# Optimization experiments

Hardware: AMD Instinct MI355X
Metric: run time of the kernel (lower is better)

The kernel has to match this reference:

```python
import jax, jax.numpy as jnp
import numpy as np

C = 256          # in_channels
CQK = C // 8     # query/key channels


def setup_inputs() -> dict:
    key = jax.random.key(0)
    ks = jax.random.split(key, 10)
    B, H, W = 4, 64, 64
    x1 = jax.random.normal(ks[0], (B, C, H, W), dtype=jnp.float32)
    x2 = jax.random.normal(ks[1], (B, C, H, W), dtype=jnp.float32)
    s = 0.05
    Wq = jax.random.normal(ks[2], (CQK, C), dtype=jnp.float32) * s
    bq = jax.random.normal(ks[3], (CQK,), dtype=jnp.float32) * s
    Wk = jax.random.normal(ks[4], (CQK, C), dtype=jnp.float32) * s
    bk = jax.random.normal(ks[5], (CQK,), dtype=jnp.float32) * s
    Wv = jax.random.normal(ks[6], (C, C), dtype=jnp.float32) * s
    bv = jax.random.normal(ks[7], (C,), dtype=jnp.float32) * s
    Wc = jax.random.normal(ks[8], (C, 2 * C), dtype=jnp.float32) * s
    bc = jax.random.normal(ks[9], (C,), dtype=jnp.float32) * s
    return {"x1": x1, "x2": x2, "Wq": Wq, "bq": bq, "Wk": Wk, "bk": bk,
            "Wv": Wv, "bv": bv, "Wc": Wc, "bc": bc}


def _proj(x_flat, Wm, b):
    # 1x1 conv == channel GEMM: [B,C,N] -> [B,Cout,N]
    return jnp.einsum('oc,bcn->bon', Wm, x_flat) + b[None, :, None]


def reference(x1, x2, Wq, bq, Wk, bk, Wv, bv, Wc, bc):
    B, Cin, H, W = x1.shape
    N = H * W
    xf1 = x1.reshape(B, Cin, N)
    xf2 = x2.reshape(B, Cin, N)
    q1 = _proj(xf1, Wq, bq)   # [B,CQK,N]
    k1 = _proj(xf1, Wk, bk)
    v1 = _proj(xf1, Wv, bv)   # [B,C,N]
    q2 = _proj(xf2, Wq, bq)
    k2 = _proj(xf2, Wk, bk)
    v2 = _proj(xf2, Wv, bv)

    def branch(q, k, v_other):
        # attn[b,i,j] = softmax_j(q[:, :, i] . k[:, :, j])
        attn = jax.nn.softmax(jnp.einsum('bci,bcj->bij', q, k), axis=2)
        # attended[b,c,i] = sum_j v_other[b,c,j] * attn[b,i,j]
        return jnp.einsum('bcj,bij->bci', v_other, attn)

    att1 = branch(q1, k1, v2).reshape(B, Cin, H, W)
    att2 = branch(q2, k2, v1).reshape(B, Cin, H, W)

    def combine(a, b_att):
        cat = jnp.concatenate((a, b_att), axis=1).reshape(B, 2 * Cin, N)
        comb = (jnp.einsum('oc,bcn->bon', Wc, cat) + bc[None, :, None]).reshape(B, Cin, H, W)
        return jnp.abs(comb).sum(axis=1, keepdims=True)

    # NOTE: original code uses x1 in BOTH combines (faithful to source)
    out1 = combine(x1, att1)
    out2 = combine(x1, att2)
    return out1, out2
```

## Files before the change

kernel.cpp:

```cpp
#include <hip/hip_runtime.h>
#include <cstdint>

#define LOG2E 1.4426950408889634f

typedef __bf16 bf16x8 __attribute__((ext_vector_type(8)));
typedef float f32x4 __attribute__((ext_vector_type(4)));

#define MFMA16(a,b,c) __builtin_amdgcn_mfma_f32_16x16x32_bf16((a),(b),(c),0,0,0)

#define LDS_BARRIER() asm volatile("s_waitcnt lgkmcnt(0)\n\ts_barrier" ::: "memory")

constexpr size_t OFF_XT = 0;
constexpr size_t OFF_QT = 8388608;
constexpr size_t OFF_KT = 9437184;
constexpr size_t OFF_V  = 10485760;
constexpr size_t OFF_WQ = 18874368;
constexpr size_t OFF_WK = 18882560;
constexpr size_t OFF_WV = 18890752;
constexpr size_t OFF_WC = 18956288;

static __device__ __forceinline__ unsigned short f2b(float a) {
  return __builtin_bit_cast(unsigned short, (__bf16)a);
}
static __device__ __forceinline__ unsigned pk2(float a, float b) {
  return ((unsigned)f2b(b) << 16) | (unsigned)f2b(a);
}

__global__ __launch_bounds__(256) void prep_kernel(
    const float* __restrict__ x1, const float* __restrict__ x2,
    const float* __restrict__ Wq, const float* __restrict__ Wk,
    const float* __restrict__ Wv, const float* __restrict__ Wc,
    short* __restrict__ ws)
{
  __shared__ float tile[64][65];
  const int tid = threadIdx.x;
  const int blk = blockIdx.x;
  if (blk < 2048) {
    const int nt = blk & 63, ct = (blk >> 6) & 3, b = (blk >> 8) & 3, inp = blk >> 10;
    const float* x = (inp ? x2 : x1) + (size_t)(b * 256 + ct * 64) * 4096 + nt * 64;
#pragma unroll
    for (int p = 0; p < 4; ++p) {
      int r = p * 16 + (tid >> 4);
      float4 v = *(const float4*)(x + (size_t)r * 4096 + (tid & 15) * 4);
      tile[r][(tid & 15) * 4 + 0] = v.x;
      tile[r][(tid & 15) * 4 + 1] = v.y;
      tile[r][(tid & 15) * 4 + 2] = v.z;
      tile[r][(tid & 15) * 4 + 3] = v.w;
    }
    __syncthreads();
    const int n = tid >> 2, c0 = (tid & 3) * 16;
    unsigned u[8];
#pragma unroll
    for (int k = 0; k < 8; ++k)
      u[k] = pk2(tile[c0 + 2 * k][n], tile[c0 + 2 * k + 1][n]);
    short* dst = ws + OFF_XT + (size_t)((inp * 4 + b) * 4096 + nt * 64 + n) * 256 + ct * 64 + c0;
    uint4 s0; s0.x = u[0]; s0.y = u[1]; s0.z = u[2]; s0.w = u[3];
    uint4 s1; s1.x = u[4]; s1.y = u[5]; s1.z = u[6]; s1.w = u[7];
    *(uint4*)(dst) = s0;
    *(uint4*)(dst + 8) = s1;
  } else {
    int idx = (blk - 2048) * 4096 + tid * 16;
    const float* src; short* dst; int off;
    if (idx < 8192)        { src = Wq; dst = ws + OFF_WQ; off = idx; }
    else if (idx < 16384)  { src = Wk; dst = ws + OFF_WK; off = idx - 8192; }
    else if (idx < 81920)  { src = Wv; dst = ws + OFF_WV; off = idx - 16384; }
    else                   { src = Wc; dst = ws + OFF_WC; off = idx - 81920; }
#pragma unroll
    for (int j = 0; j < 16; ++j) dst[off + j] = (short)f2b(src[off + j]);
  }
}

__global__ __launch_bounds__(256) void proj_qk_kernel(
    short* __restrict__ ws, const float* __restrict__ bq, const float* __restrict__ bk)
{
  const int tid = threadIdx.x, lane = tid & 63, wid = tid >> 6;
  const int g = lane >> 4, l15 = lane & 15;
  const int blk = blockIdx.x;
  const int nt = blk & 31, b = (blk >> 5) & 3, inp = blk >> 7;
  const int n0 = nt * 128 + wid * 32;

  const short* xp  = ws + OFF_XT + (size_t)(inp * 4 + b) * (4096 * 256) + (size_t)n0 * 256;
  const short* wqp = ws + OFF_WQ;
  const short* wkp = ws + OFF_WK;
  short* Qt = ws + OFF_QT + (size_t)(inp * 4 + b) * (4096 * 32);
  short* Kt = ws + OFF_KT + (size_t)(inp * 4 + b) * (4096 * 32);

  const f32x4 z4 = {0.f, 0.f, 0.f, 0.f};
  f32x4 aq[2][2], ak[2][2];
#pragma unroll
  for (int i = 0; i < 2; ++i)
#pragma unroll
    for (int j = 0; j < 2; ++j) { aq[i][j] = z4; ak[i][j] = z4; }

#pragma unroll
  for (int ks = 0; ks < 8; ++ks) {
    bf16x8 xa[2];
#pragma unroll
    for (int ns = 0; ns < 2; ++ns)
      xa[ns] = *(const bf16x8*)(xp + (size_t)(ns * 16 + l15) * 256 + ks * 32 + g * 8);
#pragma unroll
    for (int os = 0; os < 2; ++os) {
      bf16x8 wq8 = *(const bf16x8*)(wqp + (size_t)(os * 16 + l15) * 256 + ks * 32 + g * 8);
      bf16x8 wk8 = *(const bf16x8*)(wkp + (size_t)(os * 16 + l15) * 256 + ks * 32 + g * 8);
#pragma unroll
      for (int ns = 0; ns < 2; ++ns) {
        aq[ns][os] = MFMA16(xa[ns], wq8, aq[ns][os]);
        ak[ns][os] = MFMA16(xa[ns], wk8, ak[ns][os]);
      }
    }
  }
  float bqv[2], bkv[2];
#pragma unroll
  for (int os = 0; os < 2; ++os) { bqv[os] = bq[os * 16 + l15]; bkv[os] = bk[os * 16 + l15]; }
#pragma unroll
  for (int ns = 0; ns < 2; ++ns)
#pragma unroll
    for (int os = 0; os < 2; ++os)
#pragma unroll
      for (int r = 0; r < 4; ++r) {
        int n = n0 + ns * 16 + g * 4 + r;
        int o = os * 16 + l15;
        Qt[(size_t)n * 32 + o] = (short)f2b((aq[ns][os][r] + bqv[os]) * LOG2E);
        Kt[(size_t)n * 32 + o] = (short)f2b(ak[ns][os][r] + bkv[os]);
      }
}

__global__ __launch_bounds__(256) void proj_v_kernel(
    short* __restrict__ ws, const float* __restrict__ bv)
{
  const int tid = threadIdx.x, lane = tid & 63, wid = tid >> 6;
  const int g = lane >> 4, l15 = lane & 15;
  const int blk = blockIdx.x;
  const int nt = blk & 63, b = (blk >> 6) & 3, inp = blk >> 8;
  const int n0 = nt * 64;

  const short* xp  = ws + OFF_XT + (size_t)(inp * 4 + b) * (4096 * 256) + (size_t)n0 * 256;
  const short* wvp = ws + OFF_WV;
  short* Vp = ws + OFF_V + (size_t)(inp * 4 + b) * (256 * 4096);

  __shared__ __align__(16) char vl[32768];

  const f32x4 z4 = {0.f, 0.f, 0.f, 0.f};
  f32x4 acc[4][4];
#pragma unroll
  for (int i = 0; i < 4; ++i)
#pragma unroll
    for (int j = 0; j < 4; ++j) acc[i][j] = z4;

#pragma unroll
  for (int ks = 0; ks < 8; ++ks) {
    bf16x8 xa[4];
#pragma unroll
    for (int ns = 0; ns < 4; ++ns)
      xa[ns] = *(const bf16x8*)(xp + (size_t)(ns * 16 + l15) * 256 + ks * 32 + g * 8);
#pragma unroll
    for (int os = 0; os < 4; ++os) {
      bf16x8 wv8 = *(const bf16x8*)(wvp + (size_t)(wid * 64 + os * 16 + l15) * 256 + ks * 32 + g * 8);
#pragma unroll
      for (int ns = 0; ns < 4; ++ns)
        acc[os][ns] = MFMA16(wv8, xa[ns], acc[os][ns]);
    }
  }
  float bvv[4][4];
#pragma unroll
  for (int os = 0; os < 4; ++os)
#pragma unroll
    for (int r = 0; r < 4; ++r) bvv[os][r] = bv[wid * 64 + os * 16 + g * 4 + r];

  char* myl = vl + wid * 8192;
#pragma unroll
  for (int os = 0; os < 4; ++os)
#pragma unroll
    for (int ns = 0; ns < 4; ++ns)
#pragma unroll
      for (int r = 0; r < 4; ++r) {
        int o_loc = os * 16 + g * 4 + r;
        int n_loc = ns * 16 + l15;
        *(short*)(myl + o_loc * 128 + ((n_loc * 2) ^ ((o_loc & 7) << 4))) =
            (short)f2b(acc[os][ns][r] + bvv[os][r]);
      }
#pragma unroll
  for (int sc = 0; sc < 4; ++sc)
#pragma unroll
    for (int sj = 0; sj < 2; ++sj) {
      int c_loc = sc * 16 + l15;
      bf16x8 row = *(const bf16x8*)(myl + c_loc * 128 +
                                    (((unsigned)(sj * 64 + g * 16)) ^ ((c_loc & 7) << 4)));
      size_t c16 = (size_t)(wid * 4 + sc);
      size_t j32 = (size_t)(nt * 2 + sj);
      *(bf16x8*)(Vp + (c16 * 128 + j32) * 512 + lane * 8) = row;
    }
}

__global__ __launch_bounds__(256, 2) void attn_kernel(
    short* __restrict__ ws, const float* __restrict__ bc, float* __restrict__ out)
{
  const int tid = threadIdx.x, lane = tid & 63, wid = tid >> 6;
  const int g = lane >> 4, l15 = lane & 15;
  const int blk = blockIdx.x;
  const int itile = blk & 63, b = (blk >> 6) & 3, br = blk >> 8;
  const int i0 = itile * 64;

  __shared__ __align__(16) char sm[34048];
  float* l_l  = (float*)(sm + 32768);
  float* part = (float*)(sm + 33024);

  const short* Qb  = ws + OFF_QT + (size_t)(br * 4 + b) * (4096 * 32);
  const short* Kb  = ws + OFF_KT + (size_t)(br * 4 + b) * (4096 * 32);
  const short* Vb  = ws + OFF_V  + (size_t)((1 - br) * 4 + b) * (256 * 4096);
  const short* xb  = ws + OFF_XT + (size_t)b * (4096 * 256);
  const short* Wcb = ws + OFF_WC;

  const f32x4 z4 = {0.f, 0.f, 0.f, 0.f};

  bf16x8 qf = *(const bf16x8*)(Qb + (size_t)(i0 + wid * 16 + l15) * 32 + g * 8);

  f32x4 oc[4][4];
#pragma unroll
  for (int i = 0; i < 4; ++i)
#pragma unroll
    for (int j = 0; j < 4; ++j) oc[i][j] = z4;
  float l_run = 0.f;

  bf16x8 kf[2][4], va[2][2][4];
#pragma unroll
  for (int jt = 0; jt < 4; ++jt)
    kf[0][jt] = *(const bf16x8*)(Kb + (size_t)(jt * 16 + l15) * 32 + g * 8);
#pragma unroll
  for (int ks = 0; ks < 2; ++ks)
#pragma unroll
    for (int cs = 0; cs < 4; ++cs)
      va[0][ks][cs] = *(const bf16x8*)(Vb + ((size_t)(wid * 4 + cs) * 128 + ks) * 512 + lane * 8);

#define ATTN_BODY(tcur, CUR, NXT, tnxt, PB)                                              \
  do {                                                                                   \
    f32x4 st[4];                                                                         \
    _Pragma("unroll")                                                                    \
    for (int jt = 0; jt < 4; ++jt) st[jt] = MFMA16(kf[CUR][jt], qf, z4);                 \
    _Pragma("unroll")                                                                    \
    for (int jt = 0; jt < 4; ++jt)                                                       \
      kf[NXT][jt] = *(const bf16x8*)(Kb + (size_t)((tnxt) * 64 + jt * 16 + l15) * 32 + g * 8); \
    _Pragma("unroll")                                                                    \
    for (int ks = 0; ks < 2; ++ks)                                                       \
      _Pragma("unroll")                                                                  \
      for (int cs = 0; cs < 4; ++cs)                                                     \
        va[NXT][ks][cs] = *(const bf16x8*)(Vb + ((size_t)(wid * 4 + cs) * 128 +          \
                                                 (size_t)(tnxt) * 2 + ks) * 512 + lane * 8); \
    _Pragma("unroll")                                                                    \
    for (int jt = 0; jt < 4; ++jt)                                                       \
      _Pragma("unroll")                                                                  \
      for (int r = 0; r < 4; ++r) {                                                      \
        float p = exp2f(st[jt][r]);                                                      \
        st[jt][r] = p;                                                                   \
        l_run += p;                                                                      \
      }                                                                                  \
    {                                                                                    \
      char* Pl = sm + (PB) * 8192;                                                       \
      int irow = wid * 16 + l15;                                                         \
      unsigned sw = (unsigned)((irow & 7) << 4);                                         \
      _Pragma("unroll")                                                                  \
      for (int jt = 0; jt < 4; ++jt) {                                                   \
        unsigned long long u =                                                           \
            ((unsigned long long)pk2(st[jt][2], st[jt][3]) << 32) | pk2(st[jt][0], st[jt][1]); \
        *(unsigned long long*)(Pl + irow * 128 + (((unsigned)(jt * 32 + g * 8)) ^ sw)) = u; \
      }                                                                                  \
    }                                                                                    \
    LDS_BARRIER();                                                                       \
    {                                                                                    \
      const char* Pl = sm + (PB) * 8192;                                                 \
      _Pragma("unroll")                                                                  \
      for (int ks = 0; ks < 2; ++ks)                                                     \
        _Pragma("unroll")                                                                \
        for (int it = 0; it < 4; ++it) {                                                 \
          int i = it * 16 + l15;                                                         \
          bf16x8 pb = *(const bf16x8*)(Pl + i * 128 +                                    \
                                       (((unsigned)(ks * 64 + g * 16)) ^ ((i & 7) << 4))); \
          _Pragma("unroll")                                                              \
          for (int cs = 0; cs < 4; ++cs)                                                 \
            oc[cs][it] = MFMA16(va[CUR][ks][cs], pb, oc[cs][it]);                        \
        }                                                                                \
    }                                                                                    \
  } while (0)

  for (int t = 0; t < 64; t += 2) {
    ATTN_BODY(t, 0, 1, t + 1, 0);
    ATTN_BODY(t + 1, 1, 0, (t + 2 < 64) ? (t + 2) : 63, 1);
  }
#undef ATTN_BODY

  l_run += __shfl_xor(l_run, 16);
  l_run += __shfl_xor(l_run, 32);

  if (g == 0) l_l[wid * 16 + l15] = l_run;
  __syncthreads();
  float rl[4];
#pragma unroll
  for (int it = 0; it < 4; ++it) rl[it] = 1.f / l_l[it * 16 + l15];

#pragma unroll
  for (int cs = 0; cs < 4; ++cs)
#pragma unroll
    for (int it = 0; it < 4; ++it) {
      f32x4 v = oc[cs][it];
      v *= rl[it];
      int i = it * 16 + l15;
      unsigned byte = (unsigned)(i * 512) +
                      (((unsigned)((wid * 64 + cs * 16 + g * 4) * 2)) ^ ((i & 7) << 4));
      unsigned long long u = ((unsigned long long)pk2(v[2], v[3]) << 32) | pk2(v[0], v[1]);
      *(unsigned long long*)(sm + byte) = u;
    }
  __syncthreads();

  f32x4 cc[4][4];
#pragma unroll
  for (int i = 0; i < 4; ++i)
#pragma unroll
    for (int j = 0; j < 4; ++j) cc[i][j] = z4;

#pragma unroll
  for (int ks = 0; ks < 16; ++ks) {
    bf16x8 bfr[4];
#pragma unroll
    for (int ns = 0; ns < 4; ++ns) {
      int n = ns * 16 + l15;
      if (ks < 8)
        bfr[ns] = *(const bf16x8*)(xb + (size_t)(i0 + n) * 256 + ks * 32 + g * 8);
      else
        bfr[ns] = *(const bf16x8*)(sm + n * 512 +
                                   (((unsigned)((ks - 8) * 64 + g * 16)) ^ ((n & 7) << 4)));
    }
#pragma unroll
    for (int os = 0; os < 4; ++os) {
      bf16x8 af = *(const bf16x8*)(Wcb + (size_t)(wid * 64 + os * 16 + l15) * 512 + ks * 32 + g * 8);
#pragma unroll
      for (int ns = 0; ns < 4; ++ns)
        cc[os][ns] = MFMA16(af, bfr[ns], cc[os][ns]);
    }
  }
  float bcv[4][4];
#pragma unroll
  for (int os = 0; os < 4; ++os)
#pragma unroll
    for (int r = 0; r < 4; ++r) bcv[os][r] = bc[wid * 64 + os * 16 + g * 4 + r];

#pragma unroll
  for (int ns = 0; ns < 4; ++ns) {
    float tsum = 0.f;
#pragma unroll
    for (int os = 0; os < 4; ++os)
#pragma unroll
      for (int r = 0; r < 4; ++r)
        tsum += fabsf(cc[os][ns][r] + bcv[os][r]);
    tsum += __shfl_xor(tsum, 16);
    tsum += __shfl_xor(tsum, 32);
    if (g == 0) part[wid * 64 + ns * 16 + l15] = tsum;
  }
  __syncthreads();
  if (tid < 64) {
    float s = part[tid] + part[64 + tid] + part[128 + tid] + part[192 + tid];
    out[(size_t)br * 16384 + b * 4096 + i0 + tid] = s;
  }
}

extern "C" void kernel_launch(void* const* d_in, const int* in_sizes, int n_in,
                              void* d_out, int out_size, void* d_ws, size_t ws_size,
                              hipStream_t stream) {
  const float* x1 = (const float*)d_in[0];
  const float* x2 = (const float*)d_in[1];
  const float* Wq = (const float*)d_in[2];
  const float* bq = (const float*)d_in[3];
  const float* Wk = (const float*)d_in[4];
  const float* bk = (const float*)d_in[5];
  const float* Wv = (const float*)d_in[6];
  const float* bv = (const float*)d_in[7];
  const float* Wc = (const float*)d_in[8];
  const float* bc = (const float*)d_in[9];
  short* ws = (short*)d_ws;
  float* out = (float*)d_out;

  prep_kernel<<<2100, 256, 0, stream>>>(x1, x2, Wq, Wk, Wv, Wc, ws);
  proj_qk_kernel<<<256, 256, 0, stream>>>(ws, bq, bk);
  proj_v_kernel<<<512, 256, 0, stream>>>(ws, bv);
  attn_kernel<<<512, 256, 0, stream>>>(ws, bc, out);
}
```

Measured before the change: 151.0 us.

## Software-pipeline softmax exp with PV MFMA across tiles in attention loop

Restructures the attention loop so the QK scores for the next tile are computed while the PV MFMAs consume the P tile written in the previous iteration. A prologue computes and stores the first P tile, and each iteration then reads P from one LDS buffer while writing the next into the other. The intent is to hide exp and LDS-write latency behind matrix work. It also swaps exp2f for the hardware exp2 builtin and raises wave priority around the MFMA block. The K and V prefetch indices shift to match the new schedule, which adds index complexity and register pressure.

```diff
diff --git a/kernel.cpp b/kernel.cpp
--- a/kernel.cpp
+++ b/kernel.cpp
@@ -7,6 +7,7 @@
 typedef float f32x4 __attribute__((ext_vector_type(4)));
 
 #define MFMA16(a,b,c) __builtin_amdgcn_mfma_f32_16x16x32_bf16((a),(b),(c),0,0,0)
+#define EXP2(x) __builtin_amdgcn_exp2f(x)
 
 #define LDS_BARRIER() asm volatile("s_waitcnt lgkmcnt(0)\n\ts_barrier" ::: "memory")
 
@@ -212,6 +213,8 @@
   const short* Wcb = ws + OFF_WC;
 
   const f32x4 z4 = {0.f, 0.f, 0.f, 0.f};
+  const int irow = wid * 16 + l15;
+  const unsigned sw = (unsigned)((irow & 7) << 4);
 
   bf16x8 qf = *(const bf16x8*)(Qb + (size_t)(i0 + wid * 16 + l15) * 32 + g * 8);
 
@@ -222,52 +225,63 @@
     for (int j = 0; j < 4; ++j) oc[i][j] = z4;
   float l_run = 0.f;
 
+  {
+    bf16x8 kt[4];
+#pragma unroll
+    for (int jt = 0; jt < 4; ++jt)
+      kt[jt] = *(const bf16x8*)(Kb + (size_t)(jt * 16 + l15) * 32 + g * 8);
+    f32x4 s0[4];
+#pragma unroll
+    for (int jt = 0; jt < 4; ++jt) s0[jt] = MFMA16(kt[jt], qf, z4);
+#pragma unroll
+    for (int jt = 0; jt < 4; ++jt) {
+#pragma unroll
+      for (int r = 0; r < 4; ++r) {
+        float p = EXP2(s0[jt][r]);
+        s0[jt][r] = p;
+        l_run += p;
+      }
+      unsigned long long u =
+          ((unsigned long long)pk2(s0[jt][2], s0[jt][3]) << 32) | pk2(s0[jt][0], s0[jt][1]);
+      *(unsigned long long*)(sm + irow * 128 + (((unsigned)(jt * 32 + g * 8)) ^ sw)) = u;
+    }
+  }
+
   bf16x8 kf[2][4], va[2][2][4];
 #pragma unroll
   for (int jt = 0; jt < 4; ++jt)
-    kf[0][jt] = *(const bf16x8*)(Kb + (size_t)(jt * 16 + l15) * 32 + g * 8);
+    kf[0][jt] = *(const bf16x8*)(Kb + (size_t)(64 + jt * 16 + l15) * 32 + g * 8);
 #pragma unroll
   for (int ks = 0; ks < 2; ++ks)
 #pragma unroll
     for (int cs = 0; cs < 4; ++cs)
       va[0][ks][cs] = *(const bf16x8*)(Vb + ((size_t)(wid * 4 + cs) * 128 + ks) * 512 + lane * 8);
 
-#define ATTN_BODY(tcur, CUR, NXT, tnxt, PB)                                              \
+  LDS_BARRIER();
+
+#define ATTN_BODY(TC, CUR, NXT, PBR, PBW)                                                \
   do {                                                                                   \
+    const int tc = (TC);                                                                 \
+    const bool live = (tc < 63);                                                         \
     f32x4 st[4];                                                                         \
     _Pragma("unroll")                                                                    \
     for (int jt = 0; jt < 4; ++jt) st[jt] = MFMA16(kf[CUR][jt], qf, z4);                 \
-    _Pragma("unroll")                                                                    \
-    for (int jt = 0; jt < 4; ++jt)                                                       \
-      kf[NXT][jt] = *(const bf16x8*)(Kb + (size_t)((tnxt) * 64 + jt * 16 + l15) * 32 + g * 8); \
-    _Pragma("unroll")                                                                    \
-    for (int ks = 0; ks < 2; ++ks)                                                       \
+    {                                                                                    \
+      const int t2 = (tc + 2 < 64) ? tc + 2 : 63;                                        \
+      const int t1 = (tc + 1 < 64) ? tc + 1 : 63;                                        \
       _Pragma("unroll")                                                                  \
-      for (int cs = 0; cs < 4; ++cs)                                                     \
-        va[NXT][ks][cs] = *(const bf16x8*)(Vb + ((size_t)(wid * 4 + cs) * 128 +          \
-                                                 (size_t)(tnxt) * 2 + ks) * 512 + lane * 8); \
-    _Pragma("unroll")                                                                    \
-    for (int jt = 0; jt < 4; ++jt)                                                       \
+      for (int jt = 0; jt < 4; ++jt)                                                     \
+        kf[NXT][jt] = *(const bf16x8*)(Kb + (size_t)(t2 * 64 + jt * 16 + l15) * 32 + g * 8); \
       _Pragma("unroll")                                                                  \
-      for (int r = 0; r < 4; ++r) {                                                      \
-        float p = exp2f(st[jt][r]);                                                      \
-        st[jt][r] = p;                                                                   \
-        l_run += p;                                                                      \
-      }                                                                                  \
+      for (int ks = 0; ks < 2; ++ks)                                                     \
+        _Pragma("unroll")                                                                \
+        for (int cs = 0; cs < 4; ++cs)                                                   \
+          va[NXT][ks][cs] = *(const bf16x8*)(Vb + ((size_t)(wid * 4 + cs) * 128 +        \
+                                                   (size_t)t1 * 2 + ks) * 512 + lane * 8); \
+    }                                                                                    \
+    __builtin_amdgcn_s_setprio(1);                                                       \
     {                                                                                    \
-      char* Pl = sm + (PB) * 8192;                                                       \
-      int irow = wid * 16 + l15;                                                         \
-      unsigned sw = (unsigned)((irow & 7) << 4);                                         \
-      _Pragma("unroll")                                                                  \
-      for (int jt = 0; jt < 4; ++jt) {                                                   \
-        unsigned long long u =                                                           \
-            ((unsigned long long)pk2(st[jt][2], st[jt][3]) << 32) | pk2(st[jt][0], st[jt][1]); \
-        *(unsigned long long*)(Pl + irow * 128 + (((unsigned)(jt * 32 + g * 8)) ^ sw)) = u; \
-      }                                                                                  \
-    }                                                                                    \
-    LDS_BARRIER();                                                                       \
-    {                                                                                    \
-      const char* Pl = sm + (PB) * 8192;                                                 \
+      const char* Pl = sm + (PBR) * 8192;                                                \
       _Pragma("unroll")                                                                  \
       for (int ks = 0; ks < 2; ++ks)                                                     \
         _Pragma("unroll")                                                                \
@@ -280,18 +294,35 @@
             oc[cs][it] = MFMA16(va[CUR][ks][cs], pb, oc[cs][it]);                        \
         }                                                                                \
     }                                                                                    \
+    __builtin_amdgcn_s_setprio(0);                                                       \
+    if (live) {                                                                          \
+      char* Pw = sm + (PBW) * 8192;                                                      \
+      _Pragma("unroll")                                                                  \
+      for (int jt = 0; jt < 4; ++jt) {                                                   \
+        _Pragma("unroll")                                                                \
+        for (int r = 0; r < 4; ++r) {                                                    \
+          float p = EXP2(st[jt][r]);                                                     \
+          st[jt][r] = p;                                                                 \
+          l_run += p;                                                                    \
+        }                                                                                \
+        unsigned long long u =                                                           \
+            ((unsigned long long)pk2(st[jt][2], st[jt][3]) << 32) | pk2(st[jt][0], st[jt][1]); \
+        *(unsigned long long*)(Pw + irow * 128 + (((unsigned)(jt * 32 + g * 8)) ^ sw)) = u; \
+      }                                                                                  \
+    }                                                                                    \
+    LDS_BARRIER();                                                                       \
   } while (0)
 
   for (int t = 0; t < 64; t += 2) {
-    ATTN_BODY(t, 0, 1, t + 1, 0);
-    ATTN_BODY(t + 1, 1, 0, (t + 2 < 64) ? (t + 2) : 63, 1);
+    ATTN_BODY(t, 0, 1, 0, 1);
+    ATTN_BODY(t + 1, 1, 0, 1, 0);
   }
 #undef ATTN_BODY
 
   l_run += __shfl_xor(l_run, 16);
   l_run += __shfl_xor(l_run, 32);
 
-  if (g == 0) l_l[wid * 16 + l15] = l_run;
+  if (g == 0) l_l[irow] = l_run;
   __syncthreads();
   float rl[4];
 #pragma unroll
```

After: 141.1 us. 1.07x faster.
